# Kernel tuning notes

Hardware: AMD Instinct MI355X
Metric: run time of the kernel (lower is better)

The kernel has to match this reference:

```python
import jax, jax.numpy as jnp
import numpy as np

BATCH = 4096        # config['batch_size']
N_PARTS = 4         # config['n_parts']
TEMP = 0.1          # config['temp_fac']
D = 256             # embedding dim
BS = 3 * BATCH      # bs = 3 * batch_size
EPS = 1e-6          # CosineSimilarity eps


def setup_inputs() -> dict:
    key = jax.random.key(0)
    reg_pred = jax.random.normal(key, (BS, D), dtype=jnp.float32)
    return {"reg_pred": reg_pred}


def reference(reg_pred):
    B, bs, t = BATCH, BS, TEMP
    # cosine similarity: x/max(||x||, eps)
    nrm = jnp.linalg.norm(reg_pred, axis=1, keepdims=True)
    xn = reg_pred / jnp.maximum(nrm, EPS)
    E = jnp.exp((xn @ xn.T) / t)                      # exp(cos_sim/temp), [bs, bs]

    # negative-index mask: for anchor row a (pos_index p = a % B),
    # excluded indices are range(rem, bs, 4) with rem = p % n_parts
    k = jnp.arange(bs)
    rem = (k % B) % N_PARTS                           # rem per anchor row, [bs]
    excluded = (k[None, :] >= rem[:, None]) & (((k[None, :] - rem[:, None]) % 4) == 0)
    den = jnp.sum(jnp.where(excluded, 0.0, E), axis=1)  # [bs], sum exp(den sims)

    p = jnp.arange(B)
    i1, i2, i3 = p, B + p, 2 * B + p

    def pair_loss(a, b, n):
        # symmetrical NT-Xent-style term; n = exp(num_sim / t)
        return -jnp.log(n / (n + den[a])) - jnp.log(n / (n + den[b]))

    n12 = E[i1, i2]
    n13 = E[i1, i3]
    n23 = E[i2, i3]
    total = jnp.sum(pair_loss(i1, i2, n12)
                    + pair_loss(i1, i3, n13)
                    + pair_loss(i2, i3, n23))
    return total / (2 * B)
```

## Files before the change

### kernel.cpp

```cpp
#include <hip/hip_runtime.h>
#include <hip/hip_bf16.h>
#include <cstdint>
#include <cstddef>

#define BS_TOT 12288
#define DIM    256
#define BATCH_ 4096
#define NTILE  96
#define NPAIR  4656

typedef float f32x16 __attribute__((ext_vector_type(16)));
typedef int   i32x8  __attribute__((ext_vector_type(8)));

__global__ __launch_bounds__(256) void normalize_kernel(const float* __restrict__ x,
                                                        uint8_t* __restrict__ xn,
                                                        float* __restrict__ invn,
                                                        float* __restrict__ den,
                                                        float* __restrict__ out,
                                                        int osz) {
  if (blockIdx.x == 0 && (int)threadIdx.x < osz) out[threadIdx.x] = 0.0f;
  const int wave = threadIdx.x >> 6;
  const int lane = threadIdx.x & 63;
  const int row  = blockIdx.x * 4 + wave;
  const float4 v = ((const float4*)(x + (size_t)row * DIM))[lane];
  float ss = v.x*v.x + v.y*v.y + v.z*v.z + v.w*v.w;
  #pragma unroll
  for (int off = 1; off < 64; off <<= 1) ss += __shfl_xor(ss, off, 64);
  const float s = 1.0f / fmaxf(sqrtf(ss), 1e-6f);
  if (lane == 0) { invn[row] = s; den[row] = 0.0f; }
  const float sc = s * 3.79828286f;
  unsigned int w = __builtin_amdgcn_cvt_pk_fp8_f32(v.x * sc, v.y * sc, 0u, false);
  w = __builtin_amdgcn_cvt_pk_fp8_f32(v.z * sc, v.w * sc, w, true);
  ((unsigned int*)(xn + (size_t)row * DIM))[lane] = w;
}

__global__ __launch_bounds__(256, 2) void gemm_den_kernel(const uint8_t* __restrict__ xn,
                                                          float* __restrict__ den) {
  __shared__ __align__(16) uint8_t As[128 * 256];
  __shared__ __align__(16) uint8_t Bs[128 * 256];

  const int tid = threadIdx.x;

  const int t = blockIdx.x;
  int j = (int)((sqrtf(8.0f * (float)t + 1.0f) - 1.0f) * 0.5f);
  while ((j + 1) * (j + 2) / 2 <= t) j++;
  while (j * (j + 1) / 2 > t) j--;
  const int tI = t - j * (j + 1) / 2;
  const int tJ = j;
  const bool offd = (tI != tJ);

  const int wave = tid >> 6, lane = tid & 63;
  const int wr   = wave >> 1, wc = wave & 1;
  const int l31  = lane & 31, half = lane >> 5;

  const uint8_t* Ab = xn + (size_t)tI * 128 * DIM;
  const uint8_t* Bb = xn + (size_t)tJ * 128 * DIM;

  int4 chA[8], chB[8];
  #pragma unroll
  for (int c = 0; c < 8; c++) {
    const int q = c * 256 + tid;
    const size_t off = (size_t)(q >> 4) * DIM + (size_t)(q & 15) * 16;
    chA[c] = *(const int4*)(Ab + off);
    chB[c] = *(const int4*)(Bb + off);
  }
  #pragma unroll
  for (int c = 0; c < 8; c++) {
    const int q   = c * 256 + tid;
    const int row = q >> 4, k16 = q & 15;
    const int wa  = row * 256 + (((k16 >> 1) ^ (row & 7)) * 32) + (k16 & 1) * 16;
    *(int4*)(As + wa) = chA[c];
    *(int4*)(Bs + wa) = chB[c];
  }
  __syncthreads();

  const int e7 = l31 & 7;
  const int rowA0 = (wr * 64 + l31) * 256;
  const int rowB0 = (wc * 64 + l31) * 256;

  f32x16 acc[2][2]  = {};
  f32x16 accT[2][2] = {};
  #pragma unroll
  for (int ks = 0; ks < 4; ks++) {
    const int u = ((2 * ks + half) ^ e7) * 32;
    i32x8 af[2], bf[2];
    af[0] = *(const i32x8*)(As + rowA0 + u);
    af[1] = *(const i32x8*)(As + rowA0 + 32 * 256 + u);
    bf[0] = *(const i32x8*)(Bs + rowB0 + u);
    bf[1] = *(const i32x8*)(Bs + rowB0 + 32 * 256 + u);
    #pragma unroll
    for (int mi = 0; mi < 2; mi++)
      #pragma unroll
      for (int ni = 0; ni < 2; ni++)
        acc[mi][ni] = __builtin_amdgcn_mfma_scale_f32_32x32x64_f8f6f4(
            af[mi], bf[ni], acc[mi][ni], 0, 0, 0, 0x7F7F7F7F, 0, 0x7F7F7F7F);
    if (offd) {
      #pragma unroll
      for (int ni = 0; ni < 2; ni++)
        #pragma unroll
        for (int mi = 0; mi < 2; mi++)
          accT[ni][mi] = __builtin_amdgcn_mfma_scale_f32_32x32x64_f8f6f4(
              bf[ni], af[mi], accT[ni][mi], 0, 0, 0, 0x7F7F7F7F, 0, 0x7F7F7F7F);
    }
  }

  const int colBaseF = tJ * 128 + wc * 64;
  #pragma unroll
  for (int ni = 0; ni < 2; ni++) {
    float cs = 0.0f;
    #pragma unroll
    for (int mi = 0; mi < 2; mi++)
      #pragma unroll
      for (int r = 0; r < 16; r++)
        if (((l31 ^ r) & 3) != 0)
          cs += __builtin_amdgcn_exp2f(acc[mi][ni][r]);
    cs += __shfl_xor(cs, 32, 64);
    if (half == 0) atomicAdd(&den[colBaseF + ni * 32 + l31], cs);
  }
  if (offd) {
    const int colBaseT = tI * 128 + wr * 64;
    #pragma unroll
    for (int mi = 0; mi < 2; mi++) {
      float cs = 0.0f;
      #pragma unroll
      for (int ni = 0; ni < 2; ni++)
        #pragma unroll
        for (int r = 0; r < 16; r++)
          if (((l31 ^ r) & 3) != 0)
            cs += __builtin_amdgcn_exp2f(accT[ni][mi][r]);
      cs += __shfl_xor(cs, 32, 64);
      if (half == 0) atomicAdd(&den[colBaseT + mi * 32 + l31], cs);
    }
  }
}

__global__ __launch_bounds__(256) void loss_kernel(const float* __restrict__ x,
                                                   const float* __restrict__ invn,
                                                   const float* __restrict__ den,
                                                   float* __restrict__ out) {
  __shared__ float part[4];
  const int wave = threadIdx.x >> 6, lane = threadIdx.x & 63;
  const int p = blockIdx.x * 4 + wave;
  const float4 a = ((const float4*)(x + (size_t)p * DIM))[lane];
  const float4 b = ((const float4*)(x + (size_t)(BATCH_ + p) * DIM))[lane];
  const float4 c = ((const float4*)(x + (size_t)(2*BATCH_ + p) * DIM))[lane];
  float d12 = a.x*b.x + a.y*b.y + a.z*b.z + a.w*b.w;
  float d13 = a.x*c.x + a.y*c.y + a.z*c.z + a.w*c.w;
  float d23 = b.x*c.x + b.y*c.y + b.z*c.z + b.w*c.w;
  #pragma unroll
  for (int off = 1; off < 64; off <<= 1) {
    d12 += __shfl_xor(d12, off, 64);
    d13 += __shfl_xor(d13, off, 64);
    d23 += __shfl_xor(d23, off, 64);
  }
  if (lane == 0) {
    const float s1 = invn[p], s2 = invn[BATCH_ + p], s3 = invn[2*BATCH_ + p];
    const float z12 = d12 * s1 * s2 * 10.0f;
    const float z13 = d13 * s1 * s3 * 10.0f;
    const float z23 = d23 * s2 * s3 * 10.0f;
    const float n12 = __expf(z12), n13 = __expf(z13), n23 = __expf(z23);
    const float e1 = den[p], e2 = den[BATCH_ + p], e3 = den[2*BATCH_ + p];
    part[wave] = __logf(n12 + e1) + __logf(n12 + e2) - 2.0f * z12
               + __logf(n13 + e1) + __logf(n13 + e3) - 2.0f * z13
               + __logf(n23 + e2) + __logf(n23 + e3) - 2.0f * z23;
  }
  __syncthreads();
  if (threadIdx.x == 0) {
    atomicAdd(out, (part[0] + part[1] + part[2] + part[3]) * (1.0f / (2.0f * BATCH_)));
  }
}

extern "C" void kernel_launch(void* const* d_in, const int* in_sizes, int n_in,
                              void* d_out, int out_size, void* d_ws, size_t ws_size,
                              hipStream_t stream) {
  const float* x = (const float*)d_in[0];
  float* out = (float*)d_out;

  char* ws = (char*)d_ws;
  uint8_t* xn   = (uint8_t*)ws;
  float*   invn = (float*)(ws + (size_t)BS_TOT * DIM);
  float*   den  = (float*)(ws + (size_t)BS_TOT * DIM + BS_TOT * 4);

  normalize_kernel<<<BS_TOT / 4, 256, 0, stream>>>(x, xn, invn, den, out, out_size);
  gemm_den_kernel<<<NPAIR, 256, 0, stream>>>(xn, den);
  loss_kernel<<<BATCH_ / 4, 256, 0, stream>>>(x, invn, den, out);
}
```

Baseline: 122.8 us.

## Make GEMM kernel persistent and prefetch next tile pair during compute

The GEMM+exp-sum kernel becomes persistent: 512 blocks stride over the 4656 triangular tile pairs instead of one block per pair. While computing the current tile, each block issues global loads for the next pair into registers, and a custom barrier waits only on LDS so those loads stay in flight. This hides global load latency and cuts block launch overhead. The cost is more register pressure, and the 512-block grid may balance load poorly across CUs, since diagonal and off-diagonal tiles take different time.

```diff
diff --git a/kernel.cpp b/kernel.cpp
--- a/kernel.cpp
+++ b/kernel.cpp
@@ -3,11 +3,12 @@
 #include <cstdint>
 #include <cstddef>
 
-#define BS_TOT 12288
-#define DIM    256
-#define BATCH_ 4096
-#define NTILE  96
-#define NPAIR  4656
+#define BS_TOT  12288
+#define DIM     256
+#define BATCH_  4096
+#define NTILE   96
+#define NPAIR   4656
+#define NBLOCKS 512
 
 typedef float f32x16 __attribute__((ext_vector_type(16)));
 typedef int   i32x8  __attribute__((ext_vector_type(8)));
@@ -34,103 +35,137 @@
   ((unsigned int*)(xn + (size_t)row * DIM))[lane] = w;
 }
 
+__device__ __forceinline__ void decode_pair(int t, int& tI, int& tJ) {
+  int j = (int)((sqrtf(8.0f * (float)t + 1.0f) - 1.0f) * 0.5f);
+  while ((j + 1) * (j + 2) / 2 <= t) j++;
+  while (j * (j + 1) / 2 > t) j--;
+  tI = t - j * (j + 1) / 2;
+  tJ = j;
+}
+
+#define BARRIER_NO_VMDRAIN() asm volatile("s_waitcnt lgkmcnt(0)\n\ts_barrier" ::: "memory")
+
 __global__ __launch_bounds__(256, 2) void gemm_den_kernel(const uint8_t* __restrict__ xn,
                                                           float* __restrict__ den) {
   __shared__ __align__(16) uint8_t As[128 * 256];
   __shared__ __align__(16) uint8_t Bs[128 * 256];
 
-  const int tid = threadIdx.x;
-
-  const int t = blockIdx.x;
-  int j = (int)((sqrtf(8.0f * (float)t + 1.0f) - 1.0f) * 0.5f);
-  while ((j + 1) * (j + 2) / 2 <= t) j++;
-  while (j * (j + 1) / 2 > t) j--;
-  const int tI = t - j * (j + 1) / 2;
-  const int tJ = j;
-  const bool offd = (tI != tJ);
-
+  const int tid  = threadIdx.x;
   const int wave = tid >> 6, lane = tid & 63;
   const int wr   = wave >> 1, wc = wave & 1;
   const int l31  = lane & 31, half = lane >> 5;
-
-  const uint8_t* Ab = xn + (size_t)tI * 128 * DIM;
-  const uint8_t* Bb = xn + (size_t)tJ * 128 * DIM;
-
-  int4 chA[8], chB[8];
-  #pragma unroll
-  for (int c = 0; c < 8; c++) {
-    const int q = c * 256 + tid;
-    const size_t off = (size_t)(q >> 4) * DIM + (size_t)(q & 15) * 16;
-    chA[c] = *(const int4*)(Ab + off);
-    chB[c] = *(const int4*)(Bb + off);
-  }
+  const int e7   = l31 & 7;
+  const int rowA0 = (wr * 64 + l31) * 256;
+  const int rowB0 = (wc * 64 + l31) * 256;
+
+  size_t goff[8]; int wadr[8];
   #pragma unroll
   for (int c = 0; c < 8; c++) {
     const int q   = c * 256 + tid;
     const int row = q >> 4, k16 = q & 15;
-    const int wa  = row * 256 + (((k16 >> 1) ^ (row & 7)) * 32) + (k16 & 1) * 16;
-    *(int4*)(As + wa) = chA[c];
-    *(int4*)(Bs + wa) = chB[c];
-  }
-  __syncthreads();
-
-  const int e7 = l31 & 7;
-  const int rowA0 = (wr * 64 + l31) * 256;
-  const int rowB0 = (wc * 64 + l31) * 256;
-
-  f32x16 acc[2][2]  = {};
-  f32x16 accT[2][2] = {};
-  #pragma unroll
-  for (int ks = 0; ks < 4; ks++) {
-    const int u = ((2 * ks + half) ^ e7) * 32;
-    i32x8 af[2], bf[2];
-    af[0] = *(const i32x8*)(As + rowA0 + u);
-    af[1] = *(const i32x8*)(As + rowA0 + 32 * 256 + u);
-    bf[0] = *(const i32x8*)(Bs + rowB0 + u);
-    bf[1] = *(const i32x8*)(Bs + rowB0 + 32 * 256 + u);
+    goff[c] = (size_t)row * DIM + (size_t)k16 * 16;
+    wadr[c] = row * 256 + (((k16 >> 1) ^ (row & 7)) * 32) + (k16 & 1) * 16;
+  }
+
+  int tcur = blockIdx.x;
+  int tIc, tJc;
+  decode_pair(tcur, tIc, tJc);
+
+  int4 chA[8], chB[8];
+  {
+    const uint8_t* Ab = xn + (size_t)tIc * 128 * DIM;
+    const uint8_t* Bb = xn + (size_t)tJc * 128 * DIM;
     #pragma unroll
-    for (int mi = 0; mi < 2; mi++)
+    for (int c = 0; c < 8; c++) {
+      chA[c] = *(const int4*)(Ab + goff[c]);
+      chB[c] = *(const int4*)(Bb + goff[c]);
+    }
+  }
+
+  for (;;) {
+    const bool offd = (tIc != tJc);
+    const int  curI = tIc, curJ = tJc;
+
+    #pragma unroll
+    for (int c = 0; c < 8; c++) {
+      *(int4*)(As + wadr[c]) = chA[c];
+      *(int4*)(Bs + wadr[c]) = chB[c];
+    }
+    BARRIER_NO_VMDRAIN();
+
+    const int  tnext = tcur + NBLOCKS;
+    const bool more  = (tnext < NPAIR);
+    if (more) {
+      decode_pair(tnext, tIc, tJc);
+      const uint8_t* An = xn + (size_t)tIc * 128 * DIM;
+      const uint8_t* Bn = xn + (size_t)tJc * 128 * DIM;
       #pragma unroll
-      for (int ni = 0; ni < 2; ni++)
-        acc[mi][ni] = __builtin_amdgcn_mfma_scale_f32_32x32x64_f8f6f4(
-            af[mi], bf[ni], acc[mi][ni], 0, 0, 0, 0x7F7F7F7F, 0, 0x7F7F7F7F);
-    if (offd) {
+      for (int c = 0; c < 8; c++) {
+        chA[c] = *(const int4*)(An + goff[c]);
+        chB[c] = *(const int4*)(Bn + goff[c]);
+      }
+    }
+
+    f32x16 acc[2][2]  = {};
+    f32x16 accT[2][2] = {};
+    #pragma unroll
+    for (int ks = 0; ks < 4; ks++) {
+      const int u = ((2 * ks + half) ^ e7) * 32;
+      i32x8 af[2], bf[2];
+      af[0] = *(const i32x8*)(As + rowA0 + u);
+      af[1] = *(const i32x8*)(As + rowA0 + 32 * 256 + u);
+      bf[0] = *(const i32x8*)(Bs + rowB0 + u);
+      bf[1] = *(const i32x8*)(Bs + rowB0 + 32 * 256 + u);
       #pragma unroll
-      for (int ni = 0; ni < 2; ni++)
+      for (int mi = 0; mi < 2; mi++)
+        #pragma unroll
+        for (int ni = 0; ni < 2; ni++)
+          acc[mi][ni] = __builtin_amdgcn_mfma_scale_f32_32x32x64_f8f6f4(
+              af[mi], bf[ni], acc[mi][ni], 0, 0, 0, 0x7F7F7F7F, 0, 0x7F7F7F7F);
+      if (offd) {
+        #pragma unroll
+        for (int ni = 0; ni < 2; ni++)
+          #pragma unroll
+          for (int mi = 0; mi < 2; mi++)
+            accT[ni][mi] = __builtin_amdgcn_mfma_scale_f32_32x32x64_f8f6f4(
+                bf[ni], af[mi], accT[ni][mi], 0, 0, 0, 0x7F7F7F7F, 0, 0x7F7F7F7F);
+      }
+    }
+    BARRIER_NO_VMDRAIN();
+
+    {
+      const int colBaseF = curJ * 128 + wc * 64;
+      #pragma unroll
+      for (int ni = 0; ni < 2; ni++) {
+        float cs = 0.0f;
         #pragma unroll
         for (int mi = 0; mi < 2; mi++)
-          accT[ni][mi] = __builtin_amdgcn_mfma_scale_f32_32x32x64_f8f6f4(
-              bf[ni], af[mi], accT[ni][mi], 0, 0, 0, 0x7F7F7F7F, 0, 0x7F7F7F7F);
-    }
-  }
-
-  const int colBaseF = tJ * 128 + wc * 64;
-  #pragma unroll
-  for (int ni = 0; ni < 2; ni++) {
-    float cs = 0.0f;
-    #pragma unroll
-    for (int mi = 0; mi < 2; mi++)
-      #pragma unroll
-      for (int r = 0; r < 16; r++)
-        if (((l31 ^ r) & 3) != 0)
-          cs += __builtin_amdgcn_exp2f(acc[mi][ni][r]);
-    cs += __shfl_xor(cs, 32, 64);
-    if (half == 0) atomicAdd(&den[colBaseF + ni * 32 + l31], cs);
-  }
-  if (offd) {
-    const int colBaseT = tI * 128 + wr * 64;
-    #pragma unroll
-    for (int mi = 0; mi < 2; mi++) {
-      float cs = 0.0f;
-      #pragma unroll
-      for (int ni = 0; ni < 2; ni++)
-        #pragma unroll
-        for (int r = 0; r < 16; r++)
-          if (((l31 ^ r) & 3) != 0)
-            cs += __builtin_amdgcn_exp2f(accT[ni][mi][r]);
-      cs += __shfl_xor(cs, 32, 64);
-      if (half == 0) atomicAdd(&den[colBaseT + mi * 32 + l31], cs);
-    }
+          #pragma unroll
+          for (int r = 0; r < 16; r++)
+            if (((l31 ^ r) & 3) != 0)
+              cs += __builtin_amdgcn_exp2f(acc[mi][ni][r]);
+        cs += __shfl_xor(cs, 32, 64);
+        if (half == 0) atomicAdd(&den[colBaseF + ni * 32 + l31], cs);
+      }
+      if (offd) {
+        const int colBaseT = curI * 128 + wr * 64;
+        #pragma unroll
+        for (int mi = 0; mi < 2; mi++) {
+          float cs = 0.0f;
+          #pragma unroll
+          for (int ni = 0; ni < 2; ni++)
+            #pragma unroll
+            for (int r = 0; r < 16; r++)
+              if (((l31 ^ r) & 3) != 0)
+                cs += __builtin_amdgcn_exp2f(accT[ni][mi][r]);
+          cs += __shfl_xor(cs, 32, 64);
+          if (half == 0) atomicAdd(&den[colBaseT + mi * 32 + l31], cs);
+        }
+      }
+    }
+
+    if (!more) break;
+    tcur = tnext;
   }
 }
 
@@ -182,6 +217,6 @@
   float*   den  = (float*)(ws + (size_t)BS_TOT * DIM + BS_TOT * 4);
 
   normalize_kernel<<<BS_TOT / 4, 256, 0, stream>>>(x, xn, invn, den, out, out_size);
-  gemm_den_kernel<<<NPAIR, 256, 0, stream>>>(xn, den);
+  gemm_den_kernel<<<NBLOCKS, 256, 0, stream>>>(xn, den);
   loss_kernel<<<BATCH_ / 4, 256, 0, stream>>>(x, invn, den, out);
 }
```

Result: slower. 189.4 us (+54.2%).

## Make gemm_den persistent over row-major tile pairs, reusing the A tile

Applied to the files above, without the earlier changes.

Replaces one block per upper-triangular tile pair with 512 persistent blocks. Each block walks a contiguous range of pairs in row-major order, so the A tile stays in shared memory while tI is unchanged and only the B tile is reloaded. This cuts global-to-LDS traffic and per-block launch and setup overhead. In exchange, loads are no longer overlapped with compute across blocks, each tile adds barriers, and load balance is coarser because diagonal and off-diagonal pairs differ in cost.

```diff
diff --git a/kernel.cpp b/kernel.cpp
--- a/kernel.cpp
+++ b/kernel.cpp
@@ -3,11 +3,12 @@
 #include <cstdint>
 #include <cstddef>
 
-#define BS_TOT 12288
-#define DIM    256
-#define BATCH_ 4096
-#define NTILE  96
-#define NPAIR  4656
+#define BS_TOT  12288
+#define DIM     256
+#define BATCH_  4096
+#define NTILE   96
+#define NPAIR   4656
+#define NBLOCKS 512
 
 typedef float f32x16 __attribute__((ext_vector_type(16)));
 typedef int   i32x8  __attribute__((ext_vector_type(8)));
@@ -34,102 +35,125 @@
   ((unsigned int*)(xn + (size_t)row * DIM))[lane] = w;
 }
 
+__device__ __forceinline__ void decode_rowmajor(int t, int& tI, int& tJ) {
+  int i = (int)((193.0f - sqrtf(193.0f * 193.0f - 8.0f * (float)t)) * 0.5f);
+  if (i < 0) i = 0;
+  while ((i + 1) * (193 - (i + 1)) / 2 <= t) i++;
+  while (i * (193 - i) / 2 > t) i--;
+  tI = i;
+  tJ = i + (t - i * (193 - i) / 2);
+}
+
+#define BARRIER_LGKM() asm volatile("s_waitcnt lgkmcnt(0)\n\ts_barrier" ::: "memory")
+
 __global__ __launch_bounds__(256, 2) void gemm_den_kernel(const uint8_t* __restrict__ xn,
                                                           float* __restrict__ den) {
   __shared__ __align__(16) uint8_t As[128 * 256];
   __shared__ __align__(16) uint8_t Bs[128 * 256];
 
-  const int tid = threadIdx.x;
-
-  const int t = blockIdx.x;
-  int j = (int)((sqrtf(8.0f * (float)t + 1.0f) - 1.0f) * 0.5f);
-  while ((j + 1) * (j + 2) / 2 <= t) j++;
-  while (j * (j + 1) / 2 > t) j--;
-  const int tI = t - j * (j + 1) / 2;
-  const int tJ = j;
-  const bool offd = (tI != tJ);
-
+  const int tid  = threadIdx.x;
   const int wave = tid >> 6, lane = tid & 63;
   const int wr   = wave >> 1, wc = wave & 1;
   const int l31  = lane & 31, half = lane >> 5;
-
-  const uint8_t* Ab = xn + (size_t)tI * 128 * DIM;
-  const uint8_t* Bb = xn + (size_t)tJ * 128 * DIM;
-
-  int4 chA[8], chB[8];
-  #pragma unroll
-  for (int c = 0; c < 8; c++) {
-    const int q = c * 256 + tid;
-    const size_t off = (size_t)(q >> 4) * DIM + (size_t)(q & 15) * 16;
-    chA[c] = *(const int4*)(Ab + off);
-    chB[c] = *(const int4*)(Bb + off);
-  }
+  const int e7   = l31 & 7;
+  const int rowA0 = (wr * 64 + l31) * 256;
+  const int rowB0 = (wc * 64 + l31) * 256;
+
+  size_t goff[8]; int wadr[8];
   #pragma unroll
   for (int c = 0; c < 8; c++) {
     const int q   = c * 256 + tid;
     const int row = q >> 4, k16 = q & 15;
-    const int wa  = row * 256 + (((k16 >> 1) ^ (row & 7)) * 32) + (k16 & 1) * 16;
-    *(int4*)(As + wa) = chA[c];
-    *(int4*)(Bs + wa) = chB[c];
-  }
-  __syncthreads();
-
-  const int e7 = l31 & 7;
-  const int rowA0 = (wr * 64 + l31) * 256;
-  const int rowB0 = (wc * 64 + l31) * 256;
-
-  f32x16 acc[2][2]  = {};
-  f32x16 accT[2][2] = {};
-  #pragma unroll
-  for (int ks = 0; ks < 4; ks++) {
-    const int u = ((2 * ks + half) ^ e7) * 32;
-    i32x8 af[2], bf[2];
-    af[0] = *(const i32x8*)(As + rowA0 + u);
-    af[1] = *(const i32x8*)(As + rowA0 + 32 * 256 + u);
-    bf[0] = *(const i32x8*)(Bs + rowB0 + u);
-    bf[1] = *(const i32x8*)(Bs + rowB0 + 32 * 256 + u);
+    goff[c] = (size_t)row * DIM + (size_t)k16 * 16;
+    wadr[c] = row * 256 + (((k16 >> 1) ^ (row & 7)) * 32) + (k16 & 1) * 16;
+  }
+
+  const int b     = blockIdx.x;
+  const int start = (int)((long)b * NPAIR / NBLOCKS);
+  const int end   = (int)((long)(b + 1) * NPAIR / NBLOCKS);
+
+  int prevI = -1;
+  for (int t = start; t < end; t++) {
+    int tI, tJ;
+    decode_rowmajor(t, tI, tJ);
+    const bool offd = (tI != tJ);
+    const bool newA = (tI != prevI);
+    prevI = tI;
+
+    {
+      const uint8_t* Bb = xn + (size_t)tJ * 128 * DIM;
+      int4 chB[8];
+      #pragma unroll
+      for (int c = 0; c < 8; c++) chB[c] = *(const int4*)(Bb + goff[c]);
+      if (newA) {
+        const uint8_t* Ab = xn + (size_t)tI * 128 * DIM;
+        int4 chA[8];
+        #pragma unroll
+        for (int c = 0; c < 8; c++) chA[c] = *(const int4*)(Ab + goff[c]);
+        #pragma unroll
+        for (int c = 0; c < 8; c++) *(int4*)(As + wadr[c]) = chA[c];
+      }
+      #pragma unroll
+      for (int c = 0; c < 8; c++) *(int4*)(Bs + wadr[c]) = chB[c];
+    }
+    BARRIER_LGKM();
+
+    f32x16 acc[2][2]  = {};
+    f32x16 accT[2][2] = {};
     #pragma unroll
-    for (int mi = 0; mi < 2; mi++)
-      #pragma unroll
-      for (int ni = 0; ni < 2; ni++)
-        acc[mi][ni] = __builtin_amdgcn_mfma_scale_f32_32x32x64_f8f6f4(
-            af[mi], bf[ni], acc[mi][ni], 0, 0, 0, 0x7F7F7F7F, 0, 0x7F7F7F7F);
-    if (offd) {
-      #pragma unroll
-      for (int ni = 0; ni < 2; ni++)
+    for (int ks = 0; ks < 4; ks++) {
+      const int u = ((2 * ks + half) ^ e7) * 32;
+      i32x8 af[2], bf[2];
+      af[0] = *(const i32x8*)(As + rowA0 + u);
+      af[1] = *(const i32x8*)(As + rowA0 + 32 * 256 + u);
+      bf[0] = *(const i32x8*)(Bs + rowB0 + u);
+      bf[1] = *(const i32x8*)(Bs + rowB0 + 32 * 256 + u);
+      #pragma unroll
+      for (int mi = 0; mi < 2; mi++)
+        #pragma unroll
+        for (int ni = 0; ni < 2; ni++)
+          acc[mi][ni] = __builtin_amdgcn_mfma_scale_f32_32x32x64_f8f6f4(
+              af[mi], bf[ni], acc[mi][ni], 0, 0, 0, 0x7F7F7F7F, 0, 0x7F7F7F7F);
+      if (offd) {
+        #pragma unroll
+        for (int ni = 0; ni < 2; ni++)
+          #pragma unroll
+          for (int mi = 0; mi < 2; mi++)
+            accT[ni][mi] = __builtin_amdgcn_mfma_scale_f32_32x32x64_f8f6f4(
+                bf[ni], af[mi], accT[ni][mi], 0, 0, 0, 0x7F7F7F7F, 0, 0x7F7F7F7F);
+      }
+    }
+    BARRIER_LGKM();
+
+    {
+      const int colBaseF = tJ * 128 + wc * 64;
+      #pragma unroll
+      for (int ni = 0; ni < 2; ni++) {
+        float cs = 0.0f;
         #pragma unroll
         for (int mi = 0; mi < 2; mi++)
-          accT[ni][mi] = __builtin_amdgcn_mfma_scale_f32_32x32x64_f8f6f4(
-              bf[ni], af[mi], accT[ni][mi], 0, 0, 0, 0x7F7F7F7F, 0, 0x7F7F7F7F);
-    }
-  }
-
-  const int colBaseF = tJ * 128 + wc * 64;
-  #pragma unroll
-  for (int ni = 0; ni < 2; ni++) {
-    float cs = 0.0f;
-    #pragma unroll
-    for (int mi = 0; mi < 2; mi++)
-      #pragma unroll
-      for (int r = 0; r < 16; r++)
-        if (((l31 ^ r) & 3) != 0)
-          cs += __builtin_amdgcn_exp2f(acc[mi][ni][r]);
-    cs += __shfl_xor(cs, 32, 64);
-    if (half == 0) atomicAdd(&den[colBaseF + ni * 32 + l31], cs);
-  }
-  if (offd) {
-    const int colBaseT = tI * 128 + wr * 64;
-    #pragma unroll
-    for (int mi = 0; mi < 2; mi++) {
-      float cs = 0.0f;
-      #pragma unroll
-      for (int ni = 0; ni < 2; ni++)
-        #pragma unroll
-        for (int r = 0; r < 16; r++)
-          if (((l31 ^ r) & 3) != 0)
-            cs += __builtin_amdgcn_exp2f(accT[ni][mi][r]);
-      cs += __shfl_xor(cs, 32, 64);
-      if (half == 0) atomicAdd(&den[colBaseT + mi * 32 + l31], cs);
+          #pragma unroll
+          for (int r = 0; r < 16; r++)
+            if (((l31 ^ r) & 3) != 0)
+              cs += __builtin_amdgcn_exp2f(acc[mi][ni][r]);
+        cs += __shfl_xor(cs, 32, 64);
+        if (half == 0) atomicAdd(&den[colBaseF + ni * 32 + l31], cs);
+      }
+      if (offd) {
+        const int colBaseT = tI * 128 + wr * 64;
+        #pragma unroll
+        for (int mi = 0; mi < 2; mi++) {
+          float cs = 0.0f;
+          #pragma unroll
+          for (int ni = 0; ni < 2; ni++)
+            #pragma unroll
+            for (int r = 0; r < 16; r++)
+              if (((l31 ^ r) & 3) != 0)
+                cs += __builtin_amdgcn_exp2f(accT[ni][mi][r]);
+          cs += __shfl_xor(cs, 32, 64);
+          if (half == 0) atomicAdd(&den[colBaseT + mi * 32 + l31], cs);
+        }
+      }
     }
   }
 }
@@ -182,6 +206,6 @@
   float*   den  = (float*)(ws + (size_t)BS_TOT * DIM + BS_TOT * 4);
 
   normalize_kernel<<<BS_TOT / 4, 256, 0, stream>>>(x, xn, invn, den, out, out_size);
-  gemm_den_kernel<<<NPAIR, 256, 0, stream>>>(xn, den);
+  gemm_den_kernel<<<NBLOCKS, 256, 0, stream>>>(xn, den);
   loss_kernel<<<BATCH_ / 4, 256, 0, stream>>>(x, invn, den, out);
 }
```

Result: no change. 121.6 us (-1.0%).
